# Kernel optimization log

Measured on AMD Instinct MI355X. Metric: run time of the kernel, lower is better.

## Reference

```python
import jax, jax.numpy as jnp
import numpy as np

N = 50000   # nodes
HID = 32    # hidden_channels
H = 8       # heads == num_edge_features (positional-arg aliasing in source)
E = 800000  # message-passing edges
L = 100000  # supervision (label) edges
NEG_SLOPE = 0.2


def gat_layer(x, src, dst, edge_attr, W, a_src, a_dst, We, a_e, b):
    # x: [N, Fin]; W: [Fin, H*C] -> out [N, H*C] (concat heads), PyG GATConv math
    C = W.shape[1] // H
    h = (x @ W).reshape(-1, H, C)                 # [N, H, C]
    al_src = (h * a_src).sum(-1)                  # [N, H]
    al_dst = (h * a_dst).sum(-1)                  # [N, H]
    he = (edge_attr @ We).reshape(-1, H, C)       # [E, H, C]
    al_e = (he * a_e).sum(-1)                     # [E, H]
    alpha = al_src[src] + al_dst[dst] + al_e      # [E, H]
    alpha = jax.nn.leaky_relu(alpha, NEG_SLOPE)
    # segment softmax over destination-node neighborhoods
    amax = jax.ops.segment_max(alpha, dst, num_segments=N)
    amax = jnp.where(jnp.isfinite(amax), amax, 0.0)
    ex = jnp.exp(alpha - amax[dst])
    denom = jax.ops.segment_sum(ex, dst, num_segments=N)
    w = ex / (denom[dst] + 1e-16)                 # [E, H]
    out = jax.ops.segment_sum(h[src] * w[:, :, None], dst, num_segments=N)
    return out.reshape(-1, H * C) + b             # [N, H*C]


def setup_inputs():
    key = jax.random.key(0)
    ks = jax.random.split(key, 24)
    s = 0.1
    d = {}
    d["node_ids"] = jax.random.randint(ks[0], (N,), 0, N)
    d["edge_index"] = jax.random.randint(ks[1], (2, E), 0, N)
    d["edge_label_index"] = jax.random.randint(ks[2], (2, L), 0, N)
    d["topic"] = jax.random.randint(ks[3], (1,), 0, 10)
    d["edge_attr"] = jax.random.normal(ks[4], (E, H))
    d["edge_label_attr"] = jax.random.normal(ks[5], (L, H))
    d["emb"] = jax.random.normal(ks[6], (N, HID)) * s
    d["W1"] = jax.random.normal(ks[7], (HID, H * HID)) * s
    d["a_src1"] = jax.random.normal(ks[8], (H, HID)) * s
    d["a_dst1"] = jax.random.normal(ks[9], (H, HID)) * s
    d["We1"] = jax.random.normal(ks[10], (H, H * HID)) * s
    d["a_e1"] = jax.random.normal(ks[11], (H, HID)) * s
    d["b1"] = jnp.zeros((H * HID,))
    d["lin1_W"] = jax.random.normal(ks[12], (H * HID, HID)) * s
    d["lin1_b"] = jnp.zeros((HID,))
    d["W2"] = jax.random.normal(ks[13], (HID, H * HID)) * s
    d["a_src2"] = jax.random.normal(ks[14], (H, HID)) * s
    d["a_dst2"] = jax.random.normal(ks[15], (H, HID)) * s
    d["We2"] = jax.random.normal(ks[16], (H, H * HID)) * s
    d["a_e2"] = jax.random.normal(ks[17], (H, HID)) * s
    d["b2"] = jnp.zeros((H * HID,))
    d["lin5_W"] = jax.random.normal(ks[18], (H * HID, H)) * s
    d["lin5_b"] = jnp.zeros((H,))
    d["clf_W"] = jax.random.normal(ks[19], (2 * H, H)) * s
    d["clf_b"] = jnp.zeros((H,))
    return d


def reference(node_ids, edge_index, edge_label_index, topic, edge_attr, edge_label_attr, emb, W1, a_src1, a_dst1, We1, a_e1, b1, lin1_W, lin1_b, W2, a_src2, a_dst2, We2, a_e2, b2, lin5_W, lin5_b, clf_W, clf_b):
    src, dst = edge_index[0], edge_index[1]
    x = emb[node_ids]                                                   # [N, HID]
    x = jax.nn.relu(gat_layer(x, src, dst, edge_attr, W1, a_src1, a_dst1, We1, a_e1, b1))
    x = x @ lin1_W + lin1_b                                             # dropout(p=0.1) is identity in eval
    x = jax.nn.relu(gat_layer(x, src, dst, edge_attr, W2, a_src2, a_dst2, We2, a_e2, b2))
    x = x @ lin5_W + lin5_b                                             # [N, H]
    fu = x[edge_label_index[0]]                                         # [L, H]
    fm = x[edge_label_index[1]]                                         # [L, H]
    fu = jnp.concatenate([fu, edge_label_attr], axis=-1) @ clf_W + clf_b
    return jax.nn.sigmoid((fu * fm).sum(-1))                            # [L]
```

## Files before the change

kernel.cpp:

```cpp
#include <hip/hip_runtime.h>
#include <hip/hip_bf16.h>

#define HC    256
#define FIN   32
#define NH    8
#define GROUP 8
#define CAPW  32

typedef __hip_bfloat16 bf16;

__device__ __forceinline__ float blo(unsigned int u) { return __uint_as_float(u << 16); }
__device__ __forceinline__ float bhi(unsigned int u) { return __uint_as_float(u & 0xffff0000u); }
__device__ __forceinline__ unsigned int pk2(float a, float b) {
  bf16 ha = __float2bfloat16(a), hb = __float2bfloat16(b);
  unsigned short ua, ub;
  __builtin_memcpy(&ua, &ha, 2); __builtin_memcpy(&ub, &hb, 2);
  return (unsigned int)ua | ((unsigned int)ub << 16);
}

__global__ void count_kernel(const int* __restrict__ dst, int* __restrict__ cnt,
                             int* __restrict__ ord, int E_) {
  int e = blockIdx.x * blockDim.x + threadIdx.x;
  if (e < E_) ord[e] = atomicAdd(&cnt[dst[e]], 1);
}

__global__ __launch_bounds__(256) void
scan_partial(const int* __restrict__ cnt, int* __restrict__ tmp,
             int* __restrict__ bsum, int N_) {
  __shared__ int part[256];
  int t = threadIdx.x, i = blockIdx.x * 256 + t;
  int v = (i < N_) ? cnt[i] : 0;
  part[t] = v;
  __syncthreads();
#pragma unroll
  for (int off = 1; off < 256; off <<= 1) {
    int u = (t >= off) ? part[t - off] : 0;
    __syncthreads();
    part[t] += u;
    __syncthreads();
  }
  if (i < N_) tmp[i] = part[t];
  if (t == 255) bsum[blockIdx.x] = part[255];
}

__global__ __launch_bounds__(1024) void
scan_bsum_fold(int* __restrict__ bsum, int NB,
               const float* __restrict__ We1, const float* __restrict__ ae1,
               const float* __restrict__ We2, const float* __restrict__ ae2,
               const float* __restrict__ W1, const float* __restrict__ as1,
               const float* __restrict__ ad1,
               const float* __restrict__ W2, const float* __restrict__ as2,
               const float* __restrict__ ad2,
               float* __restrict__ M) {
  __shared__ int part[1024];
  int t = threadIdx.x;
  int v = (t < NB) ? bsum[t] : 0;
  part[t] = v;
  __syncthreads();
  for (int off = 1; off < 1024; off <<= 1) {
    int u = (t >= off) ? part[t - off] : 0;
    __syncthreads();
    part[t] += u;
    __syncthreads();
  }
  if (t < NB) bsum[t] = part[t] - v;

  for (int idx = t; idx < 1152; idx += 1024) {
    const float* A; const float* V; int i;
    if (idx < 64)       { i = idx;       A = We1; V = ae1; }
    else if (idx < 128) { i = idx - 64;  A = We2; V = ae2; }
    else if (idx < 384) { i = idx - 128; A = W1;  V = as1; }
    else if (idx < 640) { i = idx - 384; A = W1;  V = ad1; }
    else if (idx < 896) { i = idx - 640; A = W2;  V = as2; }
    else                { i = idx - 896; A = W2;  V = ad2; }
    int k = i >> 3, h = i & 7;
    float s = 0.f;
    for (int c = 0; c < FIN; ++c)
      s = fmaf(A[k * HC + h * FIN + c], V[h * FIN + c], s);
    M[idx] = s;
  }
}

__global__ __launch_bounds__(256) void
scan_final(const int* __restrict__ cnt, const int* __restrict__ tmp,
           const int* __restrict__ bsum, int* __restrict__ rowptr,
           int N_, int E_) {
  int t = threadIdx.x, i = blockIdx.x * 256 + t;
  if (i < N_) rowptr[i] = bsum[blockIdx.x] + tmp[i] - cnt[i];
  if (i == 0) rowptr[N_] = E_;
}

__global__ __launch_bounds__(256) void
scatter_prep_kernel(const int* __restrict__ src, const int* __restrict__ dst,
                    const int* __restrict__ rowptr, const int* __restrict__ ord,
                    int2* __restrict__ se,
                    const float* __restrict__ M,
                    const float* __restrict__ emb, const int* __restrict__ node_ids,
                    bf16* __restrict__ xq, float* __restrict__ alsrc,
                    float* __restrict__ aldst,
                    int E_, int N_, int eb) {
  __shared__ float xs[8][33];
  int t = threadIdx.x;
  if (blockIdx.x < eb) {
    int e = blockIdx.x * 256 + t;
    if (e < E_) {
      int pos = rowptr[dst[e]] + ord[e];
      se[pos] = make_int2(src[e], e);
    }
  } else {
    const float* P = M + 128;
    int n0 = (blockIdx.x - eb) * 8;
    int nl = t >> 5, c = t & 31;
    int n = n0 + nl;
    if (n < N_) {
      float v = emb[(size_t)node_ids[n] * FIN + c];
      xq[(size_t)n * FIN + c] = __float2bfloat16(v);
      xs[nl][c] = v;
    }
    __syncthreads();
    if (t < 64) {
      int nl2 = t >> 3, h = t & 7;
      int n2 = n0 + nl2;
      if (n2 < N_) {
        float sa = 0.f, sd = 0.f;
#pragma unroll
        for (int k = 0; k < FIN; ++k) {
          float x = xs[nl2][k];
          sa = fmaf(x, P[k * 8 + h], sa);
          sd = fmaf(x, P[256 + k * 8 + h], sd);
        }
        alsrc[(size_t)n2 * NH + h] = sa;
        aldst[(size_t)n2 * NH + h] = sd;
      }
    }
  }
}

__global__ __launch_bounds__(256) void
alepk_build_kernel(const int2* __restrict__ se, const float* __restrict__ edge_attr,
                   const float* __restrict__ M,
                   int* __restrict__ srcs, unsigned int* __restrict__ alepk, int E_) {
  __shared__ float Msh[128];
  int t = threadIdx.x;
  if (t < 128) Msh[t] = M[t];
  __syncthreads();
  int pos = blockIdx.x * 256 + t;
  if (pos >= E_) return;
  int2 s2 = se[pos];
  srcs[pos] = s2.x;
  int e = s2.y;
  const float4* ep = (const float4*)(edge_attr + (size_t)e * NH);
  float4 a0 = ep[0], a1 = ep[1];
  float ea[8] = {a0.x, a0.y, a0.z, a0.w, a1.x, a1.y, a1.z, a1.w};
  float o1[8], o2[8];
#pragma unroll
  for (int h = 0; h < 8; ++h) { o1[h] = 0.f; o2[h] = 0.f; }
#pragma unroll
  for (int k = 0; k < 8; ++k) {
    float x = ea[k];
#pragma unroll
    for (int h = 0; h < 8; ++h) {
      o1[h] = fmaf(x, Msh[k * 8 + h], o1[h]);
      o2[h] = fmaf(x, Msh[64 + k * 8 + h], o2[h]);
    }
  }
  uint4 r0 = make_uint4(pk2(o1[0], o1[1]), pk2(o1[2], o1[3]),
                        pk2(o1[4], o1[5]), pk2(o1[6], o1[7]));
  uint4 r1 = make_uint4(pk2(o2[0], o2[1]), pk2(o2[2], o2[3]),
                        pk2(o2[4], o2[5]), pk2(o2[6], o2[7]));
  uint4* op = (uint4*)(alepk + (size_t)pos * 8);
  op[0] = r0; op[1] = r1;
}

template <int K, int LOG2K, bool LOGITS>
__global__ __launch_bounds__(256, 8) void
agg_kernel(const int* __restrict__ rowptr, const int* __restrict__ srcs,
           const bf16* __restrict__ ale,
           const float* __restrict__ alsrc, const float* __restrict__ aldst,
           const bf16* __restrict__ xq,
           const float* __restrict__ W, const float* __restrict__ b,
           const float* __restrict__ Wlin, const float* __restrict__ blin,
           float* __restrict__ xoutf, bf16* __restrict__ xqn,
           const float* __restrict__ Pn,
           float* __restrict__ alsrcn, float* __restrict__ aldstn, int N_) {
  __shared__ __align__(16) char smem[17408];
  unsigned int* xsu = (unsigned int*)smem;
  float* wsf   = (float*)(smem + 8192);
  float* ald_s = (float*)(smem + 12288);
  float* zs   = (float*)smem;
  float* gs   = (float*)(smem + 8192);
  float* red  = (float*)smem;
  float* xrow = (float*)(smem + 16384);

  int t = threadIdx.x;
  int n0 = blockIdx.x * GROUP;
  int w = t >> 6, l = t & 63, h = l >> 3, q = l & 7;

  unsigned int* xw  = xsu + w * 512;
  float*        wsw = wsf + w * 256;
  char* xwb = smem + w * 2048;

  int nA = n0 + w * 2;
  int e0  = rowptr[(nA     <= N_) ? nA     : N_];
  int e1  = rowptr[(nA + 1 <= N_) ? nA + 1 : N_];
  int e2g = rowptr[(nA + 2 <= N_) ? nA + 2 : N_];

  if (t < GROUP * NH) {
    int nn = n0 + (t >> 3);
    ald_s[t] = (nn < N_) ? aldst[(size_t)nn * NH + (t & 7)] : 0.f;
  }
  __syncthreads();

  float4 acc0 = make_float4(0.f, 0.f, 0.f, 0.f);
  float4 acc1 = make_float4(0.f, 0.f, 0.f, 0.f);
  float dn0 = 0.f, dn1 = 0.f;

  for (int cbeg = e0; cbeg < e2g; cbeg += CAPW) {
    int clen = e2g - cbeg; if (clen > CAPW) clen = CAPW;

    {
      int el0 = (l >> 2);
      int coff = (l & 3);
      int ec0 = el0 < clen - 1 ? el0 : clen - 1;
      {
        int s = srcs[cbeg + ec0];
        const bf16* gp = xq + (size_t)s * FIN + coff * 8;
        __builtin_amdgcn_global_load_lds(
            (const __attribute__((address_space(1))) void*)gp,
            (__attribute__((address_space(3))) void*)xwb, 16, 0, 0);
      }
      if (clen > 16) {
        int el1 = 16 + el0;
        int ec1 = el1 < clen - 1 ? el1 : clen - 1;
        int s = srcs[cbeg + ec1];
        const bf16* gp = xq + (size_t)s * FIN + coff * 8;
        __builtin_amdgcn_global_load_lds(
            (const __attribute__((address_space(1))) void*)gp,
            (__attribute__((address_space(3))) void*)(xwb + 1024), 16, 0, 0);
      }
    }
    {
      int e2 = l >> 1, half = l & 1;
      if (e2 < clen) {
        int j = cbeg + e2;
        int ii = (j >= e1) ? 1 : 0;
        int sn = srcs[j];
        uint2 ue  = *(const uint2*)(ale + (size_t)j * 16 + half * 4);
        float4 as4 = *(const float4*)(alsrc + (size_t)sn * NH + half * 4);
        float4 ad4 = *(const float4*)&ald_s[(w * 2 + ii) * 8 + half * 4];
        float a0f = blo(ue.x) + as4.x + ad4.x; a0f = (a0f >= 0.f) ? a0f : 0.2f * a0f;
        float a1f = bhi(ue.x) + as4.y + ad4.y; a1f = (a1f >= 0.f) ? a1f : 0.2f * a1f;
        float a2f = blo(ue.y) + as4.z + ad4.z; a2f = (a2f >= 0.f) ? a2f : 0.2f * a2f;
        float a3f = bhi(ue.y) + as4.w + ad4.w; a3f = (a3f >= 0.f) ? a3f : 0.2f * a3f;
        *(float4*)&wsw[e2 * 8 + half * 4] =
            make_float4(__expf(a0f), __expf(a1f), __expf(a2f), __expf(a3f));
      }
    }
    asm volatile("s_waitcnt vmcnt(0) lgkmcnt(0)" ::: "memory");

    int hA = e1 - cbeg; if (hA < 0) hA = 0; if (hA > clen) hA = clen;
#pragma unroll 4
    for (int le = 0; le < hA; ++le) {
      float wv = wsw[le * 8 + h];
      uint2 u = *(const uint2*)&xw[le * 16 + q * 2];
      acc0.x = fmaf(blo(u.x), wv, acc0.x);
      acc0.y = fmaf(bhi(u.x), wv, acc0.y);
      acc0.z = fmaf(blo(u.y), wv, acc0.z);
      acc0.w = fmaf(bhi(u.y), wv, acc0.w);
      dn0 += wv;
    }
#pragma unroll 4
    for (int le = hA; le < clen; ++le) {
      float wv = wsw[le * 8 + h];
      uint2 u = *(const uint2*)&xw[le * 16 + q * 2];
      acc1.x = fmaf(blo(u.x), wv, acc1.x);
      acc1.y = fmaf(bhi(u.x), wv, acc1.y);
      acc1.z = fmaf(blo(u.y), wv, acc1.z);
      acc1.w = fmaf(bhi(u.y), wv, acc1.w);
      dn1 += wv;
    }
    asm volatile("s_waitcnt lgkmcnt(0)" ::: "memory");
  }

  float rd0 = 1.0f / (dn0 + 1e-16f);
  float rd1 = 1.0f / (dn1 + 1e-16f);
  *(float4*)&zs[(w * 2 + 0) * 256 + l * 4] =
      make_float4(acc0.x * rd0, acc0.y * rd0, acc0.z * rd0, acc0.w * rd0);
  *(float4*)&zs[(w * 2 + 1) * 256 + l * 4] =
      make_float4(acc1.x * rd1, acc1.y * rd1, acc1.z * rd1, acc1.w * rd1);
  __syncthreads();

  int hE = t >> 5;
  float g[GROUP];
#pragma unroll
  for (int i = 0; i < GROUP; ++i) g[i] = b[t];
#pragma unroll
  for (int k4 = 0; k4 < 8; ++k4) {
    float za[GROUP][4];
#pragma unroll
    for (int i = 0; i < GROUP; ++i)
      *(float4*)za[i] = *(const float4*)&zs[i * 256 + hE * 32 + k4 * 4];
#pragma unroll
    for (int kk = 0; kk < 4; ++kk) {
      float wv = W[(k4 * 4 + kk) * HC + t];
#pragma unroll
      for (int i = 0; i < GROUP; ++i) g[i] = fmaf(za[i][kk], wv, g[i]);
    }
  }
  __syncthreads();
#pragma unroll
  for (int i = 0; i < GROUP; ++i) gs[i * 256 + t] = (g[i] > 0.f) ? g[i] : 0.f;
  __syncthreads();

  {
    int kk = t & (K - 1), r = t >> LOG2K;
    float part[GROUP];
#pragma unroll
    for (int i = 0; i < GROUP; ++i) part[i] = 0.f;
#pragma unroll
    for (int j4 = 0; j4 < K / 4; ++j4) {
      float ga[GROUP][4];
#pragma unroll
      for (int i = 0; i < GROUP; ++i)
        *(float4*)ga[i] = *(const float4*)&gs[i * 256 + r * K + j4 * 4];
#pragma unroll
      for (int jj = 0; jj < 4; ++jj) {
        float wl = Wlin[(r * K + j4 * 4 + jj) * K + kk];
#pragma unroll
        for (int i = 0; i < GROUP; ++i) part[i] = fmaf(ga[i][jj], wl, part[i]);
      }
    }
#pragma unroll
    for (int i = 0; i < GROUP; ++i) red[i * 256 + t] = part[i];
  }
  __syncthreads();

  if (LOGITS) {
    if (t < GROUP * 32) {
      int i = t >> 5, kk = t & 31;
      float s = blin[kk];
#pragma unroll
      for (int r2 = 0; r2 < HC / K; ++r2) s += red[i * 256 + r2 * K + kk];
      int nn = n0 + i;
      if (nn < N_) xqn[(size_t)nn * FIN + kk] = __float2bfloat16(s);
      xrow[t] = s;
    }
    __syncthreads();
    if (t < GROUP * NH) {
      int i = t >> 3, hh = t & 7;
      int nn = n0 + i;
      if (nn < N_) {
        float sa = 0.f, sd = 0.f;
#pragma unroll
        for (int k2 = 0; k2 < FIN; ++k2) {
          float x = xrow[i * 32 + k2];
          sa = fmaf(x, Pn[k2 * 8 + hh], sa);
          sd = fmaf(x, Pn[256 + k2 * 8 + hh], sd);
        }
        alsrcn[(size_t)nn * NH + hh] = sa;
        aldstn[(size_t)nn * NH + hh] = sd;
      }
    }
  } else {
    if (t < GROUP * K) {
      int i = t >> LOG2K, kk = t & (K - 1);
      float s = blin[kk];
#pragma unroll
      for (int r2 = 0; r2 < HC / K; ++r2) s += red[i * 256 + r2 * K + kk];
      int nn = n0 + i;
      if (nn < N_) xoutf[(size_t)nn * K + kk] = s;
    }
  }
}

__global__ void clf_kernel(const int* __restrict__ eli, const float* __restrict__ ela,
                           const float* __restrict__ x2, const float* __restrict__ clfW,
                           const float* __restrict__ clfb, float* __restrict__ out, int L_) {
  int i = blockIdx.x * blockDim.x + threadIdx.x;
  if (i >= L_) return;
  int u = eli[i], m = eli[L_ + i];
  const float4* xup = (const float4*)(x2 + (size_t)u * NH);
  const float4* xmp = (const float4*)(x2 + (size_t)m * NH);
  const float4* eap = (const float4*)(ela + (size_t)i * NH);
  float4 xu0 = xup[0], xu1 = xup[1];
  float4 xm0 = xmp[0], xm1 = xmp[1];
  float4 el0 = eap[0], el1 = eap[1];
  float xu[NH] = {xu0.x, xu0.y, xu0.z, xu0.w, xu1.x, xu1.y, xu1.z, xu1.w};
  float xm[NH] = {xm0.x, xm0.y, xm0.z, xm0.w, xm1.x, xm1.y, xm1.z, xm1.w};
  float el[NH] = {el0.x, el0.y, el0.z, el0.w, el1.x, el1.y, el1.z, el1.w};
  float fu[NH];
#pragma unroll
  for (int kk = 0; kk < NH; ++kk) fu[kk] = clfb[kk];
#pragma unroll
  for (int j = 0; j < NH; ++j) {
#pragma unroll
    for (int kk = 0; kk < NH; ++kk) fu[kk] = fmaf(xu[j], clfW[j * NH + kk], fu[kk]);
  }
#pragma unroll
  for (int j = 0; j < NH; ++j) {
#pragma unroll
    for (int kk = 0; kk < NH; ++kk) fu[kk] = fmaf(el[j], clfW[(NH + j) * NH + kk], fu[kk]);
  }
  float dot = 0.f;
#pragma unroll
  for (int kk = 0; kk < NH; ++kk) dot += fu[kk] * xm[kk];
  out[i] = 1.f / (1.f + expf(-dot));
}

extern "C" void kernel_launch(void* const* d_in, const int* in_sizes, int n_in,
                              void* d_out, int out_size, void* d_ws, size_t ws_size,
                              hipStream_t stream) {
  const int* node_ids   = (const int*)d_in[0];
  const int* edge_index = (const int*)d_in[1];
  const int* eli        = (const int*)d_in[2];
  const float* edge_attr = (const float*)d_in[4];
  const float* ela       = (const float*)d_in[5];
  const float* emb       = (const float*)d_in[6];
  const float* W1     = (const float*)d_in[7];
  const float* a_src1 = (const float*)d_in[8];
  const float* a_dst1 = (const float*)d_in[9];
  const float* We1    = (const float*)d_in[10];
  const float* a_e1   = (const float*)d_in[11];
  const float* b1     = (const float*)d_in[12];
  const float* lin1W  = (const float*)d_in[13];
  const float* lin1b  = (const float*)d_in[14];
  const float* W2     = (const float*)d_in[15];
  const float* a_src2 = (const float*)d_in[16];
  const float* a_dst2 = (const float*)d_in[17];
  const float* We2    = (const float*)d_in[18];
  const float* a_e2   = (const float*)d_in[19];
  const float* b2     = (const float*)d_in[20];
  const float* lin5W  = (const float*)d_in[21];
  const float* lin5b  = (const float*)d_in[22];
  const float* clfW   = (const float*)d_in[23];
  const float* clfb   = (const float*)d_in[24];

  const int N_ = in_sizes[0];
  const int E_ = in_sizes[1] / 2;
  const int L_ = in_sizes[2] / 2;
  const int* src  = edge_index;
  const int* dstp = edge_index + E_;

  char* p = (char*)d_ws;
  auto carve = [&](size_t bytes) -> char* {
    char* r = p;
    p += (bytes + 255) & ~(size_t)255;
    return r;
  };
  bf16*  xq1     = (bf16*)carve((size_t)N_ * FIN * 2);
  bf16*  xq2     = (bf16*)carve((size_t)N_ * FIN * 2);
  unsigned int* alepk = (unsigned int*)carve((size_t)E_ * 32);
  float* alsrc1  = (float*)carve((size_t)N_ * NH * 4);
  float* aldst1  = (float*)carve((size_t)N_ * NH * 4);
  float* alsrc2  = (float*)carve((size_t)N_ * NH * 4);
  float* aldst2  = (float*)carve((size_t)N_ * NH * 4);
  float* x2b     = (float*)carve((size_t)N_ * NH * 4);
  float* Mbuf    = (float*)carve(1152 * 4);
  int*   cnt     = (int*)carve((size_t)N_ * 4);
  int*   rowptr  = (int*)carve((size_t)(N_ + 1) * 4);
  int*   stmp    = (int*)carve((size_t)N_ * 4);
  int*   bsum    = (int*)carve(1024 * 4);
  int*   srcs    = (int*)carve((size_t)E_ * 4);
  int*   ordb    = (int*)carve((size_t)E_ * 4);
  int2*  se      = (int2*)carve((size_t)E_ * 8);

  hipMemsetAsync(cnt, 0, (size_t)N_ * 4, stream);
  int eb = (E_ + 255) / 256;
  int nb = (N_ + 255) / 256;
  int pb = (N_ + 7) / 8;
  count_kernel<<<eb, 256, 0, stream>>>(dstp, cnt, ordb, E_);
  scan_partial<<<nb, 256, 0, stream>>>(cnt, stmp, bsum, N_);
  scan_bsum_fold<<<1, 1024, 0, stream>>>(bsum, nb, We1, a_e1, We2, a_e2,
                                         W1, a_src1, a_dst1, W2, a_src2, a_dst2,
                                         Mbuf);
  scan_final<<<nb, 256, 0, stream>>>(cnt, stmp, bsum, rowptr, N_, E_);
  scatter_prep_kernel<<<eb + pb, 256, 0, stream>>>(
      src, dstp, rowptr, ordb, se, Mbuf,
      emb, node_ids, xq1, alsrc1, aldst1, E_, N_, eb);
  alepk_build_kernel<<<eb, 256, 0, stream>>>(se, edge_attr, Mbuf, srcs, alepk, E_);

  int gb = (N_ + GROUP - 1) / GROUP;
  agg_kernel<32, 5, true><<<gb, 256, 0, stream>>>(
      rowptr, srcs, (const bf16*)alepk, alsrc1, aldst1, xq1,
      W1, b1, lin1W, lin1b, nullptr, xq2, Mbuf + 640, alsrc2, aldst2, N_);

  agg_kernel<8, 3, false><<<gb, 256, 0, stream>>>(
      rowptr, srcs, ((const bf16*)alepk) + 8, alsrc2, aldst2, xq2,
      W2, b2, lin5W, lin5b, x2b, nullptr, nullptr, nullptr, nullptr, N_);

  clf_kernel<<<(L_ + 255) / 256, 256, 0, stream>>>(eli, ela, x2b, clfW, clfb,
                                                   (float*)d_out, L_);
}
```

Measured before the change: 319.8 us.

## Fuse edge-attention precompute into aggregation kernels, drop alepk buffer

Removes the separate alepk_build kernel that projected edge_attr into bf16 per-edge logits and copied src ids into a compacted array. Each aggregation kernel now reads the (src, edge id) pair from the sorted se buffer, gathers the fp32 edge_attr row by original edge id, and computes the 8x8 edge-logit projection inline using a shared-memory copy of M. This saves one launch and the write/read of a 32-byte-per-edge intermediate. In exchange, each layer does a random gather of 32 bytes of edge_attr and reads 8-byte se entries instead of 4-byte srcs, and adds extra FMAs per edge in both layers.

```diff
diff --git a/kernel.cpp b/kernel.cpp
--- a/kernel.cpp
+++ b/kernel.cpp
@@ -11,12 +11,6 @@
 
 __device__ __forceinline__ float blo(unsigned int u) { return __uint_as_float(u << 16); }
 __device__ __forceinline__ float bhi(unsigned int u) { return __uint_as_float(u & 0xffff0000u); }
-__device__ __forceinline__ unsigned int pk2(float a, float b) {
-  bf16 ha = __float2bfloat16(a), hb = __float2bfloat16(b);
-  unsigned short ua, ub;
-  __builtin_memcpy(&ua, &ha, 2); __builtin_memcpy(&ub, &hb, 2);
-  return (unsigned int)ua | ((unsigned int)ub << 16);
-}
 
 __global__ void count_kernel(const int* __restrict__ dst, int* __restrict__ cnt,
                              int* __restrict__ ord, int E_) {
@@ -136,46 +130,11 @@
   }
 }
 
-__global__ __launch_bounds__(256) void
-alepk_build_kernel(const int2* __restrict__ se, const float* __restrict__ edge_attr,
-                   const float* __restrict__ M,
-                   int* __restrict__ srcs, unsigned int* __restrict__ alepk, int E_) {
-  __shared__ float Msh[128];
-  int t = threadIdx.x;
-  if (t < 128) Msh[t] = M[t];
-  __syncthreads();
-  int pos = blockIdx.x * 256 + t;
-  if (pos >= E_) return;
-  int2 s2 = se[pos];
-  srcs[pos] = s2.x;
-  int e = s2.y;
-  const float4* ep = (const float4*)(edge_attr + (size_t)e * NH);
-  float4 a0 = ep[0], a1 = ep[1];
-  float ea[8] = {a0.x, a0.y, a0.z, a0.w, a1.x, a1.y, a1.z, a1.w};
-  float o1[8], o2[8];
-#pragma unroll
-  for (int h = 0; h < 8; ++h) { o1[h] = 0.f; o2[h] = 0.f; }
-#pragma unroll
-  for (int k = 0; k < 8; ++k) {
-    float x = ea[k];
-#pragma unroll
-    for (int h = 0; h < 8; ++h) {
-      o1[h] = fmaf(x, Msh[k * 8 + h], o1[h]);
-      o2[h] = fmaf(x, Msh[64 + k * 8 + h], o2[h]);
-    }
-  }
-  uint4 r0 = make_uint4(pk2(o1[0], o1[1]), pk2(o1[2], o1[3]),
-                        pk2(o1[4], o1[5]), pk2(o1[6], o1[7]));
-  uint4 r1 = make_uint4(pk2(o2[0], o2[1]), pk2(o2[2], o2[3]),
-                        pk2(o2[4], o2[5]), pk2(o2[6], o2[7]));
-  uint4* op = (uint4*)(alepk + (size_t)pos * 8);
-  op[0] = r0; op[1] = r1;
-}
-
 template <int K, int LOG2K, bool LOGITS>
 __global__ __launch_bounds__(256, 8) void
-agg_kernel(const int* __restrict__ rowptr, const int* __restrict__ srcs,
-           const bf16* __restrict__ ale,
+agg_kernel(const int* __restrict__ rowptr, const int2* __restrict__ se,
+           const float* __restrict__ eattr,
+           const float* __restrict__ Mg,
            const float* __restrict__ alsrc, const float* __restrict__ aldst,
            const bf16* __restrict__ xq,
            const float* __restrict__ W, const float* __restrict__ b,
@@ -187,6 +146,7 @@
   unsigned int* xsu = (unsigned int*)smem;
   float* wsf   = (float*)(smem + 8192);
   float* ald_s = (float*)(smem + 12288);
+  float* Ms    = (float*)(smem + 12544);
   float* zs   = (float*)smem;
   float* gs   = (float*)(smem + 8192);
   float* red  = (float*)smem;
@@ -205,6 +165,7 @@
   int e1  = rowptr[(nA + 1 <= N_) ? nA + 1 : N_];
   int e2g = rowptr[(nA + 2 <= N_) ? nA + 2 : N_];
 
+  if (t < 64) Ms[t] = Mg[t];
   if (t < GROUP * NH) {
     int nn = n0 + (t >> 3);
     ald_s[t] = (nn < N_) ? aldst[(size_t)nn * NH + (t & 7)] : 0.f;
@@ -223,7 +184,7 @@
       int coff = (l & 3);
       int ec0 = el0 < clen - 1 ? el0 : clen - 1;
       {
-        int s = srcs[cbeg + ec0];
+        int s = se[cbeg + ec0].x;
         const bf16* gp = xq + (size_t)s * FIN + coff * 8;
         __builtin_amdgcn_global_load_lds(
             (const __attribute__((address_space(1))) void*)gp,
@@ -232,7 +193,7 @@
       if (clen > 16) {
         int el1 = 16 + el0;
         int ec1 = el1 < clen - 1 ? el1 : clen - 1;
-        int s = srcs[cbeg + ec1];
+        int s = se[cbeg + ec1].x;
         const bf16* gp = xq + (size_t)s * FIN + coff * 8;
         __builtin_amdgcn_global_load_lds(
             (const __attribute__((address_space(1))) void*)gp,
@@ -244,16 +205,31 @@
       if (e2 < clen) {
         int j = cbeg + e2;
         int ii = (j >= e1) ? 1 : 0;
-        int sn = srcs[j];
-        uint2 ue  = *(const uint2*)(ale + (size_t)j * 16 + half * 4);
-        float4 as4 = *(const float4*)(alsrc + (size_t)sn * NH + half * 4);
-        float4 ad4 = *(const float4*)&ald_s[(w * 2 + ii) * 8 + half * 4];
-        float a0f = blo(ue.x) + as4.x + ad4.x; a0f = (a0f >= 0.f) ? a0f : 0.2f * a0f;
-        float a1f = bhi(ue.x) + as4.y + ad4.y; a1f = (a1f >= 0.f) ? a1f : 0.2f * a1f;
-        float a2f = blo(ue.y) + as4.z + ad4.z; a2f = (a2f >= 0.f) ? a2f : 0.2f * a2f;
-        float a3f = bhi(ue.y) + as4.w + ad4.w; a3f = (a3f >= 0.f) ? a3f : 0.2f * a3f;
-        *(float4*)&wsw[e2 * 8 + half * 4] =
-            make_float4(__expf(a0f), __expf(a1f), __expf(a2f), __expf(a3f));
+        int2 sr = se[j];
+        int sn = sr.x, eo = sr.y;
+        float4 eah = *(const float4*)(eattr + (size_t)eo * NH + half * 4);
+        float4 ash = *(const float4*)(alsrc + (size_t)sn * NH + half * 4);
+        float eaf[4] = {eah.x, eah.y, eah.z, eah.w};
+        float ea[8];
+#pragma unroll
+        for (int c = 0; c < 4; ++c) {
+          float other = __shfl_xor(eaf[c], 1, 64);
+          ea[half * 4 + c] = eaf[c];
+          ea[(1 - half) * 4 + c] = other;
+        }
+        float asf[4] = {ash.x, ash.y, ash.z, ash.w};
+        float o[4];
+#pragma unroll
+        for (int i4 = 0; i4 < 4; ++i4) {
+          int hh = half * 4 + i4;
+          float al = 0.f;
+#pragma unroll
+          for (int kk = 0; kk < NH; ++kk) al = fmaf(ea[kk], Ms[kk * NH + hh], al);
+          float a = asf[i4] + ald_s[(w * 2 + ii) * NH + hh] + al;
+          a = (a >= 0.f) ? a : 0.2f * a;
+          o[i4] = __expf(a);
+        }
+        *(float4*)&wsw[e2 * 8 + half * 4] = make_float4(o[0], o[1], o[2], o[3]);
       }
     }
     asm volatile("s_waitcnt vmcnt(0) lgkmcnt(0)" ::: "memory");
@@ -449,7 +425,6 @@
   };
   bf16*  xq1     = (bf16*)carve((size_t)N_ * FIN * 2);
   bf16*  xq2     = (bf16*)carve((size_t)N_ * FIN * 2);
-  unsigned int* alepk = (unsigned int*)carve((size_t)E_ * 32);
   float* alsrc1  = (float*)carve((size_t)N_ * NH * 4);
   float* aldst1  = (float*)carve((size_t)N_ * NH * 4);
   float* alsrc2  = (float*)carve((size_t)N_ * NH * 4);
@@ -460,7 +435,6 @@
   int*   rowptr  = (int*)carve((size_t)(N_ + 1) * 4);
   int*   stmp    = (int*)carve((size_t)N_ * 4);
   int*   bsum    = (int*)carve(1024 * 4);
-  int*   srcs    = (int*)carve((size_t)E_ * 4);
   int*   ordb    = (int*)carve((size_t)E_ * 4);
   int2*  se      = (int2*)carve((size_t)E_ * 8);
 
@@ -477,15 +451,14 @@
   scatter_prep_kernel<<<eb + pb, 256, 0, stream>>>(
       src, dstp, rowptr, ordb, se, Mbuf,
       emb, node_ids, xq1, alsrc1, aldst1, E_, N_, eb);
-  alepk_build_kernel<<<eb, 256, 0, stream>>>(se, edge_attr, Mbuf, srcs, alepk, E_);
 
   int gb = (N_ + GROUP - 1) / GROUP;
   agg_kernel<32, 5, true><<<gb, 256, 0, stream>>>(
-      rowptr, srcs, (const bf16*)alepk, alsrc1, aldst1, xq1,
+      rowptr, se, edge_attr, Mbuf, alsrc1, aldst1, xq1,
       W1, b1, lin1W, lin1b, nullptr, xq2, Mbuf + 640, alsrc2, aldst2, N_);
 
   agg_kernel<8, 3, false><<<gb, 256, 0, stream>>>(
-      rowptr, srcs, ((const bf16*)alepk) + 8, alsrc2, aldst2, xq2,
+      rowptr, se, edge_attr, Mbuf + 64, alsrc2, aldst2, xq2,
       W2, b2, lin5W, lin5b, x2b, nullptr, nullptr, nullptr, nullptr, N_);
 
   clf_kernel<<<(L_ + 255) / 256, 256, 0, stream>>>(eli, ela, x2b, clfW, clfb,
```

After: 370.9 us. +16.0%, slower.
